# Kernel tuning notes

Hardware: AMD Instinct MI355X
Metric: run time of the kernel (lower is better)

## Reference

```python
import jax, jax.numpy as jnp
import numpy as np

N_NODES = 200000
N_EDGES = 3200000
N_GRAPHS = 64
IN_DIM, HIDDEN, OUT_DIM = 128, 16, 64


def setup_inputs() -> dict:
    key = jax.random.key(0)
    ks = jax.random.split(key, 5)
    x = jax.random.normal(ks[0], (N_NODES, IN_DIM), dtype=jnp.float32)
    edge_index = jax.random.randint(ks[1], (2, N_EDGES), 0, N_NODES, dtype=jnp.int64)
    batch = jnp.sort(jax.random.randint(ks[2], (N_NODES,), 0, N_GRAPHS, dtype=jnp.int64))
    W1 = jax.random.normal(ks[3], (IN_DIM, HIDDEN), dtype=jnp.float32) * (1.0 / np.sqrt(IN_DIM))
    W2 = jax.random.normal(ks[4], (HIDDEN, OUT_DIM), dtype=jnp.float32) * (1.0 / np.sqrt(HIDDEN))
    b1 = jnp.zeros((HIDDEN,), jnp.float32)
    b2 = jnp.zeros((OUT_DIM,), jnp.float32)
    return {"x": x, "edge_index": edge_index, "batch": batch,
            "W1": W1, "b1": b1, "W2": W2, "b2": b2, "training": 0}


def _gcn_conv(x, W, b, row, col, n_nodes):
    # PyG GCNConv: add-self-loop symmetric normalization, transform then
    # gather-from-row / scatter-add-to-col.  (row, col) already include self-loops.
    h = x @ W                                             # [N, out]
    deg = jnp.zeros((n_nodes,), h.dtype).at[col].add(1.0)  # degree incl. self-loop (>=1)
    dinv = deg ** -0.5
    norm = dinv[row] * dinv[col]                          # [E+N]
    out = jnp.zeros((n_nodes, W.shape[1]), h.dtype).at[col].add(h[row] * norm[:, None])
    return out + b


def reference(x, edge_index, batch, W1, b1, W2, b2, training):
    n = x.shape[0]
    loops = jnp.arange(n, dtype=edge_index.dtype)
    row = jnp.concatenate([edge_index[0], loops])
    col = jnp.concatenate([edge_index[1], loops])
    h = _gcn_conv(x, W1, b1, row, col, n)
    h = jax.nn.relu(h)
    # F.dropout with training=False is identity (reference is deterministic)
    h = _gcn_conv(h, W2, b2, row, col, n)
    # per-graph sum pooling: replaces the Python torch.where loop
    graph_embeds = jax.ops.segment_sum(h, batch, num_segments=N_GRAPHS)
    return graph_embeds
```

## Files before the change

kernel.cpp:

```cpp
#include <hip/hip_runtime.h>


#define TPB 256
#define CHUNK 4096
#define BK_SHIFT 9
#define NPB 512
#define W1S 20

__device__ __forceinline__ float bf2f(unsigned short u) {
    union { unsigned int i; float f; } v; v.i = ((unsigned int)u) << 16; return v.f;
}
__device__ __forceinline__ unsigned short f2bf(float f) {
    union { float f; unsigned int i; } v; v.f = f;
    unsigned int r = v.i + 0x7fff + ((v.i >> 16) & 1);
    return (unsigned short)(r >> 16);
}
__device__ __forceinline__ void bfacc8(uint4 v, float* a) {
    union { unsigned int i; float f; } lo, hi;
    lo.i = v.x << 16; hi.i = v.x & 0xffff0000u; a[0] += lo.f; a[1] += hi.f;
    lo.i = v.y << 16; hi.i = v.y & 0xffff0000u; a[2] += lo.f; a[3] += hi.f;
    lo.i = v.z << 16; hi.i = v.z & 0xffff0000u; a[4] += lo.f; a[5] += hi.f;
    lo.i = v.w << 16; hi.i = v.w & 0xffff0000u; a[6] += lo.f; a[7] += hi.f;
}
__device__ __forceinline__ void bfunp8(uint4 v, float* a) {
    union { unsigned int i; float f; } lo, hi;
    lo.i = v.x << 16; hi.i = v.x & 0xffff0000u; a[0] = lo.f; a[1] = hi.f;
    lo.i = v.y << 16; hi.i = v.y & 0xffff0000u; a[2] = lo.f; a[3] = hi.f;
    lo.i = v.z << 16; hi.i = v.z & 0xffff0000u; a[4] = lo.f; a[5] = hi.f;
    lo.i = v.w << 16; hi.i = v.w & 0xffff0000u; a[6] = lo.f; a[7] = hi.f;
}

__device__ __forceinline__ void gather32(const int* __restrict__ csr,
                                         const unsigned short* __restrict__ feat,
                                         int p, int p1, int l, int half, int sub,
                                         float* a) {
    int s_lo = csr[min(p + l, p1 - 1)];
    int s_hi = csr[min(p + 16 + l, p1 - 1)];
    int rem = p1 - p;
    int e0 = sub, e1 = 8 + sub, e2 = 16 + sub, e3 = 24 + sub;
    int src0 = __shfl(s_lo, e0, 16);
    int src1 = __shfl(s_lo, e1, 16);
    int src2 = __shfl(s_hi, e0, 16);
    int src3 = __shfl(s_hi, e1, 16);
    uint4 u0 = make_uint4(0, 0, 0, 0), u1 = make_uint4(0, 0, 0, 0);
    uint4 u2 = make_uint4(0, 0, 0, 0), u3 = make_uint4(0, 0, 0, 0);
    if (e0 < rem) u0 = *(const uint4*)&feat[(size_t)src0 * 16 + 8 * half];
    if (e1 < rem) u1 = *(const uint4*)&feat[(size_t)src1 * 16 + 8 * half];
    if (e2 < rem) u2 = *(const uint4*)&feat[(size_t)src2 * 16 + 8 * half];
    if (e3 < rem) u3 = *(const uint4*)&feat[(size_t)src3 * 16 + 8 * half];
    bfacc8(u0, a);
    bfacc8(u1, a);
    bfacc8(u2, a);
    bfacc8(u3, a);
}

__device__ __forceinline__ void gather32_pair(const int* __restrict__ csr,
                                              const unsigned short* __restrict__ feat,
                                              int pA, int pA1, int pB, int pB1,
                                              int l, int half, int sub,
                                              float* a, float* b) {
    int sAlo = csr[min(pA + l, pA1 - 1)];
    int sAhi = csr[min(pA + 16 + l, pA1 - 1)];
    int sBlo = csr[min(pB + l, pB1 - 1)];
    int sBhi = csr[min(pB + 16 + l, pB1 - 1)];
    int remA = pA1 - pA, remB = pB1 - pB;
    int e0 = sub, e1 = 8 + sub, e2 = 16 + sub, e3 = 24 + sub;
    int sa0 = __shfl(sAlo, e0, 16), sa1 = __shfl(sAlo, e1, 16);
    int sa2 = __shfl(sAhi, e0, 16), sa3 = __shfl(sAhi, e1, 16);
    int sb0 = __shfl(sBlo, e0, 16), sb1 = __shfl(sBlo, e1, 16);
    int sb2 = __shfl(sBhi, e0, 16), sb3 = __shfl(sBhi, e1, 16);
    uint4 uA0 = make_uint4(0,0,0,0), uA1 = make_uint4(0,0,0,0);
    uint4 uA2 = make_uint4(0,0,0,0), uA3 = make_uint4(0,0,0,0);
    uint4 uB0 = make_uint4(0,0,0,0), uB1 = make_uint4(0,0,0,0);
    uint4 uB2 = make_uint4(0,0,0,0), uB3 = make_uint4(0,0,0,0);
    if (e0 < remA) uA0 = *(const uint4*)&feat[(size_t)sa0 * 16 + 8 * half];
    if (e1 < remA) uA1 = *(const uint4*)&feat[(size_t)sa1 * 16 + 8 * half];
    if (e2 < remA) uA2 = *(const uint4*)&feat[(size_t)sa2 * 16 + 8 * half];
    if (e3 < remA) uA3 = *(const uint4*)&feat[(size_t)sa3 * 16 + 8 * half];
    if (e0 < remB) uB0 = *(const uint4*)&feat[(size_t)sb0 * 16 + 8 * half];
    if (e1 < remB) uB1 = *(const uint4*)&feat[(size_t)sb1 * 16 + 8 * half];
    if (e2 < remB) uB2 = *(const uint4*)&feat[(size_t)sb2 * 16 + 8 * half];
    if (e3 < remB) uB3 = *(const uint4*)&feat[(size_t)sb3 * 16 + 8 * half];
    bfacc8(uA0, a); bfacc8(uA1, a); bfacc8(uA2, a); bfacc8(uA3, a);
    bfacc8(uB0, b); bfacc8(uB1, b); bfacc8(uB2, b); bfacc8(uB3, b);
}

__global__ __launch_bounds__(TPB) void hist_kernel(const int* __restrict__ col,
                                                   int* __restrict__ counts,
                                                   int E, int nblk, int nbuck) {
    __shared__ int hist[512];
    int t = threadIdx.x;
    for (int i = t; i < nbuck; i += TPB) hist[i] = 0;
    __syncthreads();
    int e0 = blockIdx.x * CHUNK;
    for (int i = t; i < CHUNK; i += TPB) {
        int e = e0 + i;
        if (e < E) atomicAdd(&hist[col[e] >> BK_SHIFT], 1);
    }
    __syncthreads();
    for (int i = t; i < nbuck; i += TPB) counts[i * nblk + blockIdx.x] = hist[i];
}

__global__ __launch_bounds__(TPB) void scan1_kernel(const int* __restrict__ in,
                                                    int* __restrict__ out,
                                                    int* __restrict__ bsum, int L) {
    __shared__ int s[TPB];
    int t = threadIdx.x;
    int i = blockIdx.x * TPB + t;
    int d = (i < L) ? in[i] : 0;
    s[t] = d; __syncthreads();
    for (int off = 1; off < TPB; off <<= 1) {
        int v = (t >= off) ? s[t - off] : 0;
        __syncthreads();
        s[t] += v;
        __syncthreads();
    }
    if (i < L) out[i] = s[t] - d;
    if (t == TPB - 1) bsum[blockIdx.x] = s[t];
}

__global__ __launch_bounds__(1024) void scan2_kernel(int* __restrict__ bsum, int nb) {
    __shared__ int s[1024];
    int t = threadIdx.x;
    int i0 = t * 2, i1 = t * 2 + 1;
    int v0 = (i0 < nb) ? bsum[i0] : 0;
    int v1 = (i1 < nb) ? bsum[i1] : 0;
    int pv = v0 + v1;
    s[t] = pv; __syncthreads();
    for (int off = 1; off < 1024; off <<= 1) {
        int u = (t >= off) ? s[t - off] : 0;
        __syncthreads();
        s[t] += u;
        __syncthreads();
    }
    int exc = s[t] - pv;
    if (i0 < nb) bsum[i0] = exc;
    if (i1 < nb) bsum[i1] = exc + v0;
}

__device__ __forceinline__ int cbase_at(const int* counts, const int* bsum, int f) {
    return counts[f] + bsum[f >> 8];
}

__global__ __launch_bounds__(TPB) void s1c_gemm_kernel(
        const int* __restrict__ row, const int* __restrict__ col,
        const int* __restrict__ counts, const int* __restrict__ bsum,
        int E, int nblk, int nbuck,
        int* __restrict__ bucketed,
        const float* __restrict__ x, const float* __restrict__ W1,
        unsigned short* __restrict__ h1b, int N, int nbg) {
    __shared__ __align__(16) char sbuf[2048 + 2048 + 8192 + 64];
    int* slhist = (int*)sbuf;
    int* sgd    = (int*)(sbuf + 2048);
    unsigned short* ssidx = (unsigned short*)(sbuf + 4096);
    int* swtot  = (int*)(sbuf + 4096 + 8192);
    float* w1s  = (float*)sbuf;

    int b = (int)blockIdx.x, t = threadIdx.x;
    int M = min(nblk, nbg);
    int role, id;
    if (b < 2 * M) { role = b & 1; id = b >> 1; }
    else           { role = (nblk > nbg) ? 0 : 1; id = b - M; }

    if (role == 0) {
        int e0 = id * CHUNK;
        int nE = min(CHUNK, E - e0);
        int Ltot = nbuck * nblk;
        int lane = t & 63, w = t >> 6;
        int bk0 = 2 * t, bk1 = 2 * t + 1;
        int cb0 = 0, cb1 = 0, c0 = 0, c1 = 0;
        if (bk0 < nbuck) {
            int f = bk0 * nblk + id;
            cb0 = cbase_at(counts, bsum, f);
            int nx = (f + 1 < Ltot) ? cbase_at(counts, bsum, f + 1) : E;
            c0 = nx - cb0;
        }
        if (bk1 < nbuck) {
            int f = bk1 * nblk + id;
            cb1 = cbase_at(counts, bsum, f);
            int nx = (f + 1 < Ltot) ? cbase_at(counts, bsum, f + 1) : E;
            c1 = nx - cb1;
        }
        int s = c0 + c1;
        int v = s;
#pragma unroll
        for (int d = 1; d < 64; d <<= 1) {
            int u2 = __shfl_up(v, d, 64);
            if (lane >= d) v += u2;
        }
        if (lane == 63) swtot[w] = v;
        __syncthreads();
        int wbase = 0;
#pragma unroll
        for (int i = 0; i < 4; ++i) wbase += (i < w) ? swtot[i] : 0;
        int o0 = wbase + v - s;
        int o1 = o0 + c0;
        if (bk0 < nbuck) { slhist[bk0] = o0; sgd[bk0] = cb0 - o0; }
        if (bk1 < nbuck) { slhist[bk1] = o1; sgd[bk1] = cb1 - o1; }
        __syncthreads();
        for (int i = t; i < nE; i += TPB) {
            int c = col[e0 + i];
            int lp = atomicAdd(&slhist[c >> BK_SHIFT], 1);
            ssidx[lp] = (unsigned short)i;
        }
        __syncthreads();
        for (int j = t; j < nE; j += TPB) {
            int i = ssidx[j];
            int c = col[e0 + i];
            int r = row[e0 + i];
            bucketed[sgd[c >> BK_SHIFT] + j] = ((c & (NPB - 1)) << 18) | r;
        }
        return;
    }
    for (int i = t; i < 128 * 16; i += TPB)
        w1s[(i >> 4) * W1S + (i & 15)] = W1[i];
    __syncthreads();
    int g = t >> 2, q = t & 3;
    int nA = id * 128 + g;
    int nB = nA + 64;
    int nAc = min(nA, N - 1), nBc = min(nB, N - 1);
    const float4* xA = (const float4*)(x + (size_t)nAc * 128);
    const float4* xB = (const float4*)(x + (size_t)nBc * 128);
    float4 xvA[8], xvB[8];
#pragma unroll
    for (int i = 0; i < 8; ++i) xvA[i] = xA[i * 4 + q];
#pragma unroll
    for (int i = 0; i < 8; ++i) xvB[i] = xB[i * 4 + q];
    float accA[16], accB[16];
#pragma unroll
    for (int k = 0; k < 16; ++k) { accA[k] = 0.f; accB[k] = 0.f; }
#pragma unroll
    for (int i = 0; i < 8; ++i) {
        float xjA[4] = {xvA[i].x, xvA[i].y, xvA[i].z, xvA[i].w};
        float xjB[4] = {xvB[i].x, xvB[i].y, xvB[i].z, xvB[i].w};
#pragma unroll
        for (int j = 0; j < 4; ++j) {
            int k = i * 16 + q * 4 + j;
            const float4* w4 = (const float4*)&w1s[k * W1S];
            float4 wa = w4[0], wb = w4[1], wc = w4[2], wd = w4[3];
            float xa = xjA[j], xb = xjB[j];
            accA[0]  = fmaf(xa, wa.x, accA[0]);  accA[1]  = fmaf(xa, wa.y, accA[1]);
            accA[2]  = fmaf(xa, wa.z, accA[2]);  accA[3]  = fmaf(xa, wa.w, accA[3]);
            accA[4]  = fmaf(xa, wb.x, accA[4]);  accA[5]  = fmaf(xa, wb.y, accA[5]);
            accA[6]  = fmaf(xa, wb.z, accA[6]);  accA[7]  = fmaf(xa, wb.w, accA[7]);
            accA[8]  = fmaf(xa, wc.x, accA[8]);  accA[9]  = fmaf(xa, wc.y, accA[9]);
            accA[10] = fmaf(xa, wc.z, accA[10]); accA[11] = fmaf(xa, wc.w, accA[11]);
            accA[12] = fmaf(xa, wd.x, accA[12]); accA[13] = fmaf(xa, wd.y, accA[13]);
            accA[14] = fmaf(xa, wd.z, accA[14]); accA[15] = fmaf(xa, wd.w, accA[15]);
            accB[0]  = fmaf(xb, wa.x, accB[0]);  accB[1]  = fmaf(xb, wa.y, accB[1]);
            accB[2]  = fmaf(xb, wa.z, accB[2]);  accB[3]  = fmaf(xb, wa.w, accB[3]);
            accB[4]  = fmaf(xb, wb.x, accB[4]);  accB[5]  = fmaf(xb, wb.y, accB[5]);
            accB[6]  = fmaf(xb, wb.z, accB[6]);  accB[7]  = fmaf(xb, wb.w, accB[7]);
            accB[8]  = fmaf(xb, wc.x, accB[8]);  accB[9]  = fmaf(xb, wc.y, accB[9]);
            accB[10] = fmaf(xb, wc.z, accB[10]); accB[11] = fmaf(xb, wc.w, accB[11]);
            accB[12] = fmaf(xb, wd.x, accB[12]); accB[13] = fmaf(xb, wd.y, accB[13]);
            accB[14] = fmaf(xb, wd.z, accB[14]); accB[15] = fmaf(xb, wd.w, accB[15]);
        }
    }
#pragma unroll
    for (int d = 1; d < 4; d <<= 1) {
#pragma unroll
        for (int k = 0; k < 16; ++k) {
            accA[k] += __shfl_xor(accA[k], d, 4);
            accB[k] += __shfl_xor(accB[k], d, 4);
        }
    }
    if (nA < N) {
        unsigned int u0 = (unsigned int)f2bf(accA[4 * q]) |
                          ((unsigned int)f2bf(accA[4 * q + 1]) << 16);
        unsigned int u1 = (unsigned int)f2bf(accA[4 * q + 2]) |
                          ((unsigned int)f2bf(accA[4 * q + 3]) << 16);
        *(uint2*)&h1b[(size_t)nA * 16 + 4 * q] = make_uint2(u0, u1);
    }
    if (nB < N) {
        unsigned int u0 = (unsigned int)f2bf(accB[4 * q]) |
                          ((unsigned int)f2bf(accB[4 * q + 1]) << 16);
        unsigned int u1 = (unsigned int)f2bf(accB[4 * q + 2]) |
                          ((unsigned int)f2bf(accB[4 * q + 3]) << 16);
        *(uint2*)&h1b[(size_t)nB * 16 + 4 * q] = make_uint2(u0, u1);
    }
}

__global__ __launch_bounds__(TPB) void sort_kernel(
        const int* __restrict__ bucketed,
        const int* __restrict__ counts, const int* __restrict__ bsum,
        int E, int nblk, int nbuck,
        int* __restrict__ csr, int* __restrict__ offs, float* __restrict__ dinv,
        const unsigned short* __restrict__ h1b, unsigned short* __restrict__ h1p, int N) {
    __shared__ int lhist[NPB];
    __shared__ int part[TPB];
    __shared__ float sdinv[NPB];
    int bk = blockIdx.x, t = threadIdx.x;
    int n0 = bk << BK_SHIFT;
    int n1 = min(n0 + NPB, N);
    int e0 = cbase_at(counts, bsum, bk * nblk);
    int e1 = (bk + 1 < nbuck) ? cbase_at(counts, bsum, (bk + 1) * nblk) : E;

    lhist[t] = 0; lhist[t + TPB] = 0;
    __syncthreads();
    for (int i = e0 + t; i < e1; i += TPB)
        atomicAdd(&lhist[bucketed[i] >> 18], 1);
    __syncthreads();

    int base = t * 2;
    int c0 = lhist[base], c1 = lhist[base + 1];
    int s = c0 + c1;
    part[t] = s;
    __syncthreads();
    for (int off = 1; off < TPB; off <<= 1) {
        int v = (t >= off) ? part[t - off] : 0;
        __syncthreads();
        part[t] += v;
        __syncthreads();
    }
    int o0 = e0 + part[t] - s;
    int o1 = o0 + c0;
    lhist[base] = o0; lhist[base + 1] = o1;
    sdinv[base]     = rsqrtf((float)c0 + 1.0f);
    sdinv[base + 1] = rsqrtf((float)c1 + 1.0f);
    int n = n0 + base;
    if (n + 0 < N) { offs[n + 0] = o0; dinv[n + 0] = sdinv[base]; }
    if (n + 1 < N) { offs[n + 1] = o1; dinv[n + 1] = sdinv[base + 1]; }
    __syncthreads();

    for (int i = e0 + t; i < e1; i += TPB) {
        int v = bucketed[i];
        int pos = atomicAdd(&lhist[v >> 18], 1);
        csr[pos] = v & 0x3FFFF;
    }
    int nq = (n1 - n0) * 4;
    for (int i = t; i < nq; i += TPB) {
        float dv = sdinv[i >> 2];
        uint2 u = ((const uint2*)h1b)[(size_t)n0 * 4 + i];
        float f0 = bf2f((unsigned short)(u.x & 0xffff));
        float f1 = bf2f((unsigned short)(u.x >> 16));
        float f2 = bf2f((unsigned short)(u.y & 0xffff));
        float f3 = bf2f((unsigned short)(u.y >> 16));
        ((ushort4*)h1p)[(size_t)n0 * 4 + i] =
            make_ushort4(f2bf(f0 * dv), f2bf(f1 * dv), f2bf(f2 * dv), f2bf(f3 * dv));
    }
    if (bk == 0 && t == 0) offs[N] = E;
}

__global__ __launch_bounds__(TPB) void gather1_kernel(const int* __restrict__ csr,
                                                      const int* __restrict__ offs,
                                                      const unsigned short* __restrict__ h1p,
                                                      const float* __restrict__ dinv,
                                                      const float* __restrict__ b1,
                                                      unsigned short* __restrict__ h2p, int N) {
    int t = threadIdx.x;
    int grp = t >> 4, l = t & 15;
    int half = l & 1;
    int sub  = l >> 1;
    int cA = blockIdx.x * 32 + grp * 2;
    int cB = cA + 1;
    if (cA >= N) return;
    bool hasB = cB < N;
    int pA = offs[cA], pA1 = offs[cA + 1];
    int pB = hasB ? offs[cB] : 0;
    int pB1 = hasB ? offs[cB + 1] : 0;
    float a[8], bb[8];
#pragma unroll
    for (int k = 0; k < 8; ++k) { a[k] = 0.f; bb[k] = 0.f; }
    while (pA < pA1 && pB < pB1) {
        gather32_pair(csr, h1p, pA, pA1, pB, pB1, l, half, sub, a, bb);
        pA += 32; pB += 32;
    }
    while (pA < pA1) { gather32(csr, h1p, pA, pA1, l, half, sub, a); pA += 32; }
    while (pB < pB1) { gather32(csr, h1p, pB, pB1, l, half, sub, bb); pB += 32; }
#pragma unroll
    for (int d = 2; d < 16; d <<= 1) {
#pragma unroll
        for (int k = 0; k < 8; ++k) {
            a[k]  += __shfl_xor(a[k], d, 16);
            bb[k] += __shfl_xor(bb[k], d, 16);
        }
    }
    if (l < 2) {
#pragma unroll
        for (int side = 0; side < 2; ++side) {
            int c = side ? cB : cA;
            float* av = side ? bb : a;
            if (side && !hasB) break;
            float dc = dinv[c];
            uint4 sv = *(const uint4*)&h1p[(size_t)c * 16 + 8 * l];
            float sf[8];
            bfunp8(sv, sf);
            unsigned int uo[4];
#pragma unroll
            for (int q = 0; q < 4; ++q) {
                float r0 = fmaf(dc, av[2 * q] + sf[2 * q], b1[8 * l + 2 * q]);
                float r1 = fmaf(dc, av[2 * q + 1] + sf[2 * q + 1], b1[8 * l + 2 * q + 1]);
                r0 = dc * fmaxf(r0, 0.f);
                r1 = dc * fmaxf(r1, 0.f);
                uo[q] = (unsigned int)f2bf(r0) | ((unsigned int)f2bf(r1) << 16);
            }
            *(uint4*)&h2p[(size_t)c * 16 + 8 * l] = make_uint4(uo[0], uo[1], uo[2], uo[3]);
        }
    }
}

__global__ __launch_bounds__(TPB) void gather2f_kernel(
        const int* __restrict__ csr, const int* __restrict__ offs,
        const unsigned short* __restrict__ h2p, const float* __restrict__ dinv,
        const float* __restrict__ W2, const float* __restrict__ b2,
        const int* __restrict__ batch, float* __restrict__ out, int N) {
    __shared__ float w2s[16 * 64];
    __shared__ float asT[64 * 17];
    __shared__ float pool[64];
    int t = threadIdx.x;
    for (int i = t; i < 16 * 64; i += TPB) w2s[i] = W2[i];
    if (t < 64) pool[t] = 0.f;

    int n0 = blockIdx.x * 64;
    int nLast = min(n0 + 63, N - 1);
    int g0 = batch[n0];
    bool uniform = (batch[nLast] == g0);

    int grp = t >> 4, l = t & 15;
    int half = l & 1, sub = l >> 1;
#pragma unroll 1
    for (int itp = 0; itp < 2; ++itp) {
        int mA = grp * 4 + itp * 2;
        int mB = mA + 1;
        int cA = n0 + mA, cB = n0 + mB;
        if (cA < N) {
            bool hasB = cB < N;
            int pA = offs[cA], pA1 = offs[cA + 1];
            int pB = hasB ? offs[cB] : 0;
            int pB1 = hasB ? offs[cB + 1] : 0;
            float a[8], bb[8];
#pragma unroll
            for (int k = 0; k < 8; ++k) { a[k] = 0.f; bb[k] = 0.f; }
            while (pA < pA1 && pB < pB1) {
                gather32_pair(csr, h2p, pA, pA1, pB, pB1, l, half, sub, a, bb);
                pA += 32; pB += 32;
            }
            while (pA < pA1) { gather32(csr, h2p, pA, pA1, l, half, sub, a); pA += 32; }
            while (pB < pB1) { gather32(csr, h2p, pB, pB1, l, half, sub, bb); pB += 32; }
#pragma unroll
            for (int d = 2; d < 16; d <<= 1) {
#pragma unroll
                for (int k = 0; k < 8; ++k) {
                    a[k]  += __shfl_xor(a[k], d, 16);
                    bb[k] += __shfl_xor(bb[k], d, 16);
                }
            }
            if (l < 2) {
#pragma unroll
                for (int side = 0; side < 2; ++side) {
                    int c = side ? cB : cA;
                    int m = side ? mB : mA;
                    float* av = side ? bb : a;
                    if (side && !hasB) break;
                    float dc = dinv[c];
                    uint4 sv = *(const uint4*)&h2p[(size_t)c * 16 + 8 * l];
                    float sf[8];
                    bfunp8(sv, sf);
#pragma unroll
                    for (int k = 0; k < 8; ++k)
                        asT[m * 17 + 8 * l + k] = dc * (av[k] + sf[k]);
                }
            }
        }
    }
    __syncthreads();

    int wave = t >> 6, j = t & 63;
    float w2reg[16];
#pragma unroll
    for (int kx = 0; kx < 16; ++kx) w2reg[kx] = w2s[kx * 64 + j];
    float b2j = b2[j];
    float val = 0.f;
    int g_cur = -1;
#pragma unroll 1
    for (int mi = 0; mi < 16; ++mi) {
        int m = wave * 16 + mi;
        int c = n0 + m;
        if (c >= N) break;
        const float* ar = &asT[m * 17];
        float y = b2j;
#pragma unroll
        for (int kx = 0; kx < 16; ++kx) y = fmaf(ar[kx], w2reg[kx], y);
        if (uniform) {
            val += y;
        } else {
            int g = batch[c];
            if (g != g_cur) {
                if (g_cur >= 0) atomicAdd(&out[(size_t)g_cur * 64 + j], val);
                val = 0.f;
                g_cur = g;
            }
            val += y;
        }
    }
    if (uniform) {
        atomicAdd(&pool[j], val);
        __syncthreads();
        if (t < 64) atomicAdd(&out[(size_t)g0 * 64 + t], pool[t]);
    } else {
        if (g_cur >= 0) atomicAdd(&out[(size_t)g_cur * 64 + j], val);
    }
}

static inline size_t align64(size_t v) { return (v + 63) & ~(size_t)63; }

extern "C" void kernel_launch(void* const* d_in, const int* in_sizes, int n_in,
                              void* d_out, int out_size, void* d_ws, size_t ws_size,
                              hipStream_t stream) {
    const float* x     = (const float*)d_in[0];
    const int*   ei    = (const int*)d_in[1];
    const int*   batch = (const int*)d_in[2];
    const float* W1    = (const float*)d_in[3];
    const float* b1    = (const float*)d_in[4];
    const float* W2    = (const float*)d_in[5];
    const float* b2    = (const float*)d_in[6];

    const int N = in_sizes[0] / 128;
    const int E = in_sizes[1] / 2;
    const int* row = ei;
    const int* col = ei + E;

    const int NBLK  = (E + CHUNK - 1) / CHUNK;
    const int NBUCK = (N + NPB - 1) / NPB;
    const int L     = NBUCK * NBLK;
    const int NBS   = (L + TPB - 1) / TPB;
    const int NBG   = (N + 127) / 128;

    char* p = (char*)d_ws;
    int*            counts   = (int*)p;            p += align64((size_t)L * 4);
    int*            bsum     = (int*)p;            p += align64(2048 * 4);
    int*            bucketed = (int*)p;            p += align64((size_t)E * 4);
    int*            csr      = (int*)p;            p += align64((size_t)E * 4);
    int*            offs     = (int*)p;            p += align64((size_t)(N + 1) * 4);
    float*          dinv     = (float*)p;          p += align64((size_t)N * 4);
    unsigned short* h1b      = (unsigned short*)p; p += align64((size_t)N * 16 * 2);
    unsigned short* h1p      = (unsigned short*)p; p += align64((size_t)N * 16 * 2);
    unsigned short* h2p      = (unsigned short*)p; p += align64((size_t)N * 16 * 2);
    float*          out      = (float*)d_out;

    hipMemsetAsync(out, 0, (size_t)out_size * sizeof(float), stream);

    hist_kernel<<<NBLK, TPB, 0, stream>>>(col, counts, E, NBLK, NBUCK);
    scan1_kernel<<<NBS, TPB, 0, stream>>>(counts, counts, bsum, L);
    scan2_kernel<<<1, 1024, 0, stream>>>(bsum, NBS);
    s1c_gemm_kernel<<<NBLK + NBG, TPB, 0, stream>>>(row, col, counts, bsum,
                                                    E, NBLK, NBUCK,
                                                    bucketed, x, W1, h1b, N, NBG);
    sort_kernel<<<NBUCK, TPB, 0, stream>>>(bucketed, counts, bsum, E, NBLK, NBUCK,
                                           csr, offs, dinv, h1b, h1p, N);
    gather1_kernel<<<(N + 31) / 32, TPB, 0, stream>>>(csr, offs, h1p, dinv, b1, h2p, N);
    gather2f_kernel<<<(N + 63) / 64, TPB, 0, stream>>>(csr, offs, h2p, dinv,
                                                       W2, b2, batch, out, N);
}
```

Before: 329.8 us.

## Replace per-block count matrix scan with global bucket totals and atomic cursors

Blocks now add their bucket histograms into a padded global total array, and a single small kernel scans those totals. The scatter kernel recomputes its local histogram and claims output ranges through atomic cursors. This drops the two-level scan over the large block-by-bucket count matrix and one launch, and the edge chunk size is doubled. In exchange, order within a bucket is no longer deterministic, which the later per-bucket sort should absorb, and it adds global atomics plus a second histogram pass over col.

After: 367.1 us. 11.3% more time.

```diff
diff --git a/kernel.cpp b/kernel.cpp
--- a/kernel.cpp
+++ b/kernel.cpp
@@ -2,10 +2,11 @@
 
 
 #define TPB 256
-#define CHUNK 4096
+#define CHUNK 8192
 #define BK_SHIFT 9
 #define NPB 512
 #define W1S 20
+#define CPAD 16
 
 __device__ __forceinline__ float bf2f(unsigned short u) {
     union { unsigned int i; float f; } v; v.i = ((unsigned int)u) << 16; return v.f;
@@ -86,101 +87,74 @@
 }
 
 __global__ __launch_bounds__(TPB) void hist_kernel(const int* __restrict__ col,
-                                                   int* __restrict__ counts,
-                                                   int E, int nblk, int nbuck) {
+                                                   int* __restrict__ btot,
+                                                   int E, int nbuck) {
     __shared__ int hist[512];
     int t = threadIdx.x;
-    for (int i = t; i < nbuck; i += TPB) hist[i] = 0;
+    hist[t] = 0; hist[t + TPB] = 0;
     __syncthreads();
     int e0 = blockIdx.x * CHUNK;
-    for (int i = t; i < CHUNK; i += TPB) {
-        int e = e0 + i;
-        if (e < E) atomicAdd(&hist[col[e] >> BK_SHIFT], 1);
-    }
-    __syncthreads();
-    for (int i = t; i < nbuck; i += TPB) counts[i * nblk + blockIdx.x] = hist[i];
-}
-
-__global__ __launch_bounds__(TPB) void scan1_kernel(const int* __restrict__ in,
-                                                    int* __restrict__ out,
-                                                    int* __restrict__ bsum, int L) {
+    int nE = min(CHUNK, E - e0);
+    for (int i = t; i < nE; i += TPB)
+        atomicAdd(&hist[col[e0 + i] >> BK_SHIFT], 1);
+    __syncthreads();
+    for (int i = t; i < nbuck; i += TPB)
+        if (hist[i]) atomicAdd(&btot[i * CPAD], hist[i]);
+}
+
+__global__ __launch_bounds__(TPB) void bscan_kernel(const int* __restrict__ btot,
+                                                    int* __restrict__ bstart,
+                                                    int* __restrict__ cursor,
+                                                    int nbuck, int E) {
     __shared__ int s[TPB];
     int t = threadIdx.x;
-    int i = blockIdx.x * TPB + t;
-    int d = (i < L) ? in[i] : 0;
-    s[t] = d; __syncthreads();
-    for (int off = 1; off < TPB; off <<= 1) {
-        int v = (t >= off) ? s[t - off] : 0;
-        __syncthreads();
-        s[t] += v;
-        __syncthreads();
-    }
-    if (i < L) out[i] = s[t] - d;
-    if (t == TPB - 1) bsum[blockIdx.x] = s[t];
-}
-
-__global__ __launch_bounds__(1024) void scan2_kernel(int* __restrict__ bsum, int nb) {
-    __shared__ int s[1024];
-    int t = threadIdx.x;
-    int i0 = t * 2, i1 = t * 2 + 1;
-    int v0 = (i0 < nb) ? bsum[i0] : 0;
-    int v1 = (i1 < nb) ? bsum[i1] : 0;
+    int i0 = 2 * t, i1 = 2 * t + 1;
+    int v0 = (i0 < nbuck) ? btot[i0 * CPAD] : 0;
+    int v1 = (i1 < nbuck) ? btot[i1 * CPAD] : 0;
     int pv = v0 + v1;
     s[t] = pv; __syncthreads();
-    for (int off = 1; off < 1024; off <<= 1) {
+    for (int off = 1; off < TPB; off <<= 1) {
         int u = (t >= off) ? s[t - off] : 0;
         __syncthreads();
         s[t] += u;
         __syncthreads();
     }
     int exc = s[t] - pv;
-    if (i0 < nb) bsum[i0] = exc;
-    if (i1 < nb) bsum[i1] = exc + v0;
-}
-
-__device__ __forceinline__ int cbase_at(const int* counts, const int* bsum, int f) {
-    return counts[f] + bsum[f >> 8];
+    if (i0 < nbuck) { bstart[i0] = exc;      cursor[i0 * CPAD] = exc; }
+    if (i1 < nbuck) { bstart[i1] = exc + v0; cursor[i1 * CPAD] = exc + v0; }
+    if (t == 0) bstart[nbuck] = E;
 }
 
 __global__ __launch_bounds__(TPB) void s1c_gemm_kernel(
         const int* __restrict__ row, const int* __restrict__ col,
-        const int* __restrict__ counts, const int* __restrict__ bsum,
-        int E, int nblk, int nbuck,
+        int* __restrict__ cursor, int E, int nbuck,
         int* __restrict__ bucketed,
         const float* __restrict__ x, const float* __restrict__ W1,
-        unsigned short* __restrict__ h1b, int N, int nbg) {
-    __shared__ __align__(16) char sbuf[2048 + 2048 + 8192 + 64];
+        unsigned short* __restrict__ h1b, int N, int ns, int ng) {
+    __shared__ __align__(16) char sbuf[2048 + 2048 + CHUNK * 2 + 64];
     int* slhist = (int*)sbuf;
     int* sgd    = (int*)(sbuf + 2048);
     unsigned short* ssidx = (unsigned short*)(sbuf + 4096);
-    int* swtot  = (int*)(sbuf + 4096 + 8192);
+    int* swtot  = (int*)(sbuf + 4096 + CHUNK * 2);
     float* w1s  = (float*)sbuf;
 
     int b = (int)blockIdx.x, t = threadIdx.x;
-    int M = min(nblk, nbg);
+    int M = min(ns, ng);
     int role, id;
     if (b < 2 * M) { role = b & 1; id = b >> 1; }
-    else           { role = (nblk > nbg) ? 0 : 1; id = b - M; }
+    else           { role = (ns > ng) ? 0 : 1; id = b - M; }
 
     if (role == 0) {
         int e0 = id * CHUNK;
         int nE = min(CHUNK, E - e0);
-        int Ltot = nbuck * nblk;
         int lane = t & 63, w = t >> 6;
         int bk0 = 2 * t, bk1 = 2 * t + 1;
-        int cb0 = 0, cb1 = 0, c0 = 0, c1 = 0;
-        if (bk0 < nbuck) {
-            int f = bk0 * nblk + id;
-            cb0 = cbase_at(counts, bsum, f);
-            int nx = (f + 1 < Ltot) ? cbase_at(counts, bsum, f + 1) : E;
-            c0 = nx - cb0;
-        }
-        if (bk1 < nbuck) {
-            int f = bk1 * nblk + id;
-            cb1 = cbase_at(counts, bsum, f);
-            int nx = (f + 1 < Ltot) ? cbase_at(counts, bsum, f + 1) : E;
-            c1 = nx - cb1;
-        }
+        slhist[t] = 0; slhist[t + TPB] = 0;
+        __syncthreads();
+        for (int i = t; i < nE; i += TPB)
+            atomicAdd(&slhist[col[e0 + i] >> BK_SHIFT], 1);
+        __syncthreads();
+        int c0 = slhist[bk0], c1 = slhist[bk1];
         int s = c0 + c1;
         int v = s;
 #pragma unroll
@@ -189,14 +163,16 @@
             if (lane >= d) v += u2;
         }
         if (lane == 63) swtot[w] = v;
+        int gb0 = (bk0 < nbuck && c0 > 0) ? atomicAdd(&cursor[bk0 * CPAD], c0) : 0;
+        int gb1 = (bk1 < nbuck && c1 > 0) ? atomicAdd(&cursor[bk1 * CPAD], c1) : 0;
         __syncthreads();
         int wbase = 0;
 #pragma unroll
         for (int i = 0; i < 4; ++i) wbase += (i < w) ? swtot[i] : 0;
         int o0 = wbase + v - s;
         int o1 = o0 + c0;
-        if (bk0 < nbuck) { slhist[bk0] = o0; sgd[bk0] = cb0 - o0; }
-        if (bk1 < nbuck) { slhist[bk1] = o1; sgd[bk1] = cb1 - o1; }
+        slhist[bk0] = o0; sgd[bk0] = gb0 - o0;
+        slhist[bk1] = o1; sgd[bk1] = gb1 - o1;
         __syncthreads();
         for (int i = t; i < nE; i += TPB) {
             int c = col[e0 + i];
@@ -282,9 +258,8 @@
 }
 
 __global__ __launch_bounds__(TPB) void sort_kernel(
-        const int* __restrict__ bucketed,
-        const int* __restrict__ counts, const int* __restrict__ bsum,
-        int E, int nblk, int nbuck,
+        const int* __restrict__ bucketed, const int* __restrict__ bstart,
+        int E, int nbuck,
         int* __restrict__ csr, int* __restrict__ offs, float* __restrict__ dinv,
         const unsigned short* __restrict__ h1b, unsigned short* __restrict__ h1p, int N) {
     __shared__ int lhist[NPB];
@@ -293,8 +268,8 @@
     int bk = blockIdx.x, t = threadIdx.x;
     int n0 = bk << BK_SHIFT;
     int n1 = min(n0 + NPB, N);
-    int e0 = cbase_at(counts, bsum, bk * nblk);
-    int e1 = (bk + 1 < nbuck) ? cbase_at(counts, bsum, (bk + 1) * nblk) : E;
+    int e0 = bstart[bk];
+    int e1 = bstart[bk + 1];
 
     lhist[t] = 0; lhist[t + TPB] = 0;
     __syncthreads();
@@ -523,13 +498,12 @@
 
     const int NBLK  = (E + CHUNK - 1) / CHUNK;
     const int NBUCK = (N + NPB - 1) / NPB;
-    const int L     = NBUCK * NBLK;
-    const int NBS   = (L + TPB - 1) / TPB;
     const int NBG   = (N + 127) / 128;
 
     char* p = (char*)d_ws;
-    int*            counts   = (int*)p;            p += align64((size_t)L * 4);
-    int*            bsum     = (int*)p;            p += align64(2048 * 4);
+    int*            btot     = (int*)p;            p += align64(512 * CPAD * 4);
+    int*            cursor   = (int*)p;            p += align64(512 * CPAD * 4);
+    int*            bstart   = (int*)p;            p += align64(520 * 4);
     int*            bucketed = (int*)p;            p += align64((size_t)E * 4);
     int*            csr      = (int*)p;            p += align64((size_t)E * 4);
     int*            offs     = (int*)p;            p += align64((size_t)(N + 1) * 4);
@@ -540,14 +514,14 @@
     float*          out      = (float*)d_out;
 
     hipMemsetAsync(out, 0, (size_t)out_size * sizeof(float), stream);
-
-    hist_kernel<<<NBLK, TPB, 0, stream>>>(col, counts, E, NBLK, NBUCK);
-    scan1_kernel<<<NBS, TPB, 0, stream>>>(counts, counts, bsum, L);
-    scan2_kernel<<<1, 1024, 0, stream>>>(bsum, NBS);
-    s1c_gemm_kernel<<<NBLK + NBG, TPB, 0, stream>>>(row, col, counts, bsum,
-                                                    E, NBLK, NBUCK,
-                                                    bucketed, x, W1, h1b, N, NBG);
-    sort_kernel<<<NBUCK, TPB, 0, stream>>>(bucketed, counts, bsum, E, NBLK, NBUCK,
+    hipMemsetAsync(btot, 0, 512 * CPAD * 4, stream);
+
+    hist_kernel<<<NBLK, TPB, 0, stream>>>(col, btot, E, NBUCK);
+    bscan_kernel<<<1, TPB, 0, stream>>>(btot, bstart, cursor, NBUCK, E);
+    s1c_gemm_kernel<<<NBLK + NBG, TPB, 0, stream>>>(row, col, cursor, E, NBUCK,
+                                                    bucketed, x, W1, h1b, N,
+                                                    NBLK, NBG);
+    sort_kernel<<<NBUCK, TPB, 0, stream>>>(bucketed, bstart, E, NBUCK,
                                            csr, offs, dinv, h1b, h1p, N);
     gather1_kernel<<<(N + 31) / 32, TPB, 0, stream>>>(csr, offs, h1p, dinv, b1, h2p, N);
     gather2f_kernel<<<(N + 63) / 64, TPB, 0, stream>>>(csr, offs, h2p, dinv,
```
